# Kernel optimization log

Hardware: AMD Instinct MI355X
Metric: run time of the kernel (lower is better)

The kernel has to match this reference:

```python
import jax, jax.numpy as jnp
import numpy as np

B, T, C = 4, 2048, 1024
H, D = 16, 64  # num_heads, head_dim
SCALE = D ** -0.5


def setup_inputs() -> dict:
    key = jax.random.key(0)
    ks = jax.random.split(key, 6)
    s = 0.02
    return {
        "hidden_states": jax.random.normal(ks[0], (B, T, C), dtype=jnp.float32),
        "wq": jax.random.normal(ks[1], (C, C), dtype=jnp.float32) * s,
        "wk": jax.random.normal(ks[2], (C, C), dtype=jnp.float32) * s,
        "wv": jax.random.normal(ks[3], (C, C), dtype=jnp.float32) * s,
        "wo": jax.random.normal(ks[4], (C, C), dtype=jnp.float32) * s,
        "bo": jnp.zeros((C,), dtype=jnp.float32),
    }


def reference(hidden_states, wq, wk, wv, wo, bo):
    b, t, c = hidden_states.shape
    # torch nn.Linear: y = x @ W^T
    q = hidden_states @ wq.T
    k = hidden_states @ wk.T
    v = hidden_states @ wv.T
    # (b, t, c) -> (b, h, t, d)
    q = q.reshape(b, t, H, D).transpose(0, 2, 1, 3)
    k = k.reshape(b, t, H, D).transpose(0, 2, 1, 3)
    v = v.reshape(b, t, H, D).transpose(0, 2, 1, 3)
    scores = jnp.einsum("bhqd,bhkd->bhqk", q, k) * SCALE
    attn = jax.nn.softmax(scores, axis=-1)
    out = jnp.einsum("bhqk,bhkd->bhqd", attn, v)
    out = out.transpose(0, 2, 1, 3).reshape(b, t, c)
    return out @ wo.T + bo
```

## Files before the change

### kernel.cpp

```cpp
#include <hip/hip_runtime.h>
#include <hip/hip_bf16.h>
#include <stdint.h>
#include <math.h>

#define Bb 4
#define Tt 2048
#define Cc 1024
#define Hh 16
#define Dd 64
#define Mm (Bb * Tt)
#define KVB 64
#define NT (Tt / KVB)

typedef __attribute__((ext_vector_type(8))) short bf8;
typedef __attribute__((ext_vector_type(4))) float f32x4;
typedef __attribute__((ext_vector_type(16))) float f32x16;
typedef __attribute__((ext_vector_type(8))) float f32x8v;
typedef __attribute__((ext_vector_type(2))) float f32x2v;
typedef __attribute__((ext_vector_type(8))) unsigned short u16x8;

#define QSCALE 0.1803368801111244f
#define M_FIX 4.0f

__device__ __forceinline__ unsigned short f2bf(float f) {
  __hip_bfloat16 h = __float2bfloat16(f);
  return *reinterpret_cast<unsigned short*>(&h);
}
__device__ __forceinline__ float bf2f(unsigned short s) {
  union { unsigned u; float f; } v; v.u = ((unsigned)s) << 16;
  return v.f;
}
__device__ __forceinline__ float fexp2(float x) {
#if __has_builtin(__builtin_amdgcn_exp2f)
  return __builtin_amdgcn_exp2f(x);
#else
  return exp2f(x);
#endif
}
__device__ __forceinline__ unsigned cvtpk(float lo, float hi) {
  unsigned r;
  asm volatile("v_cvt_pk_bf16_f32 %0, %1, %2" : "=v"(r) : "v"(lo), "v"(hi));
  return r;
}
__device__ __forceinline__ void gl_lds16(const void* g, void* l) {
  __builtin_amdgcn_global_load_lds(
      (const __attribute__((address_space(1))) void*)g,
      (__attribute__((address_space(3))) void*)l, 16, 0, 0);
}

__global__ __launch_bounds__(256) void cast_all(
    const float* __restrict__ hs, const float* __restrict__ wq,
    const float* __restrict__ wk, const float* __restrict__ wv,
    const float* __restrict__ wo, unsigned short* __restrict__ Xb,
    unsigned short* __restrict__ Wbase) {
  long long g = (long long)(blockIdx.x * 256 + threadIdx.x) * 8;
  const float* src;
  unsigned short* dst;
  long long off;
  const long long HS = 8LL * 1024 * 1024;
  if (g < HS) {
    src = hs; dst = Xb; off = g;
  } else {
    long long r = g - HS;
    int wsel = (int)(r >> 20);
    off = r & ((1LL << 20) - 1);
    src = (wsel == 0) ? wq : (wsel == 1) ? wk : (wsel == 2) ? wv : wo;
    dst = Wbase + ((long long)wsel << 20);
  }
  const float4* p = (const float4*)(src + off);
  float4 a = p[0], b = p[1];
  u16x8 o;
  o[0] = f2bf(a.x); o[1] = f2bf(a.y); o[2] = f2bf(a.z); o[3] = f2bf(a.w);
  o[4] = f2bf(b.x); o[5] = f2bf(b.y); o[6] = f2bf(b.z); o[7] = f2bf(b.w);
  *(u16x8*)(dst + off) = o;
}

template <int MODE>
__global__ __launch_bounds__(256, 2)
void gemm_bt(const unsigned short* __restrict__ A,
             const unsigned short* __restrict__ Bw,
             void* __restrict__ Cout,
             const float* __restrict__ bias,
             int M, int N, int K) {
  __shared__ unsigned short smem[3 * 8192];
  const int tid = threadIdx.x;
  const int lane = tid & 63;
  const int w = tid >> 6;
  const int wr = w >> 1, wc = w & 1;
  const int row0 = blockIdx.y * 128;
  const int col0 = blockIdx.x * 128;
  const int lr = lane & 15;
  const int lk = (lane >> 4) * 8;

  f32x4 acc[4][4] = {};

  const int sr = tid >> 2;
  const int sc = (tid & 3) * 8;
  const int NK = K >> 5;

  const unsigned short* a0p = A  + (size_t)(row0 + sr) * K + sc;
  const unsigned short* a1p = A  + (size_t)(row0 + 64 + sr) * K + sc;
  const unsigned short* b0p = Bw + (size_t)(col0 + sr) * K + sc;
  const unsigned short* b1p = Bw + (size_t)(col0 + 64 + sr) * K + sc;

#define STAGE(kt, buf)                                                   \
  {                                                                      \
    unsigned short* As_ = &smem[(buf) * 8192];                           \
    unsigned short* Bs_ = &smem[(buf) * 8192 + 4096];                    \
    const int k0_ = (kt) * 32;                                           \
    gl_lds16(a0p + k0_, &As_[sr * 32 + sc]);                             \
    gl_lds16(a1p + k0_, &As_[(64 + sr) * 32 + sc]);                      \
    gl_lds16(b0p + k0_, &Bs_[sr * 32 + sc]);                             \
    gl_lds16(b1p + k0_, &Bs_[(64 + sr) * 32 + sc]);                      \
  }

  STAGE(0, 0)
  STAGE(1, 1)
  asm volatile("s_waitcnt vmcnt(4)" ::: "memory");
  __builtin_amdgcn_sched_barrier(0);
  __builtin_amdgcn_s_barrier();
  __builtin_amdgcn_sched_barrier(0);

  int cur = 0;
  for (int t = 0; t < NK; ++t) {
    if (t + 2 < NK) {
      int nb = cur + 2; if (nb >= 3) nb -= 3;
      STAGE(t + 2, nb)
    }
    const unsigned short* As_ = &smem[cur * 8192];
    const unsigned short* Bs_ = &smem[cur * 8192 + 4096];

    bf8 a[4], b[4];
#pragma unroll
    for (int mi = 0; mi < 4; ++mi)
      a[mi] = *(const bf8*)&As_[(wr * 64 + mi * 16 + lr) * 32 + lk];
#pragma unroll
    for (int ni = 0; ni < 4; ++ni)
      b[ni] = *(const bf8*)&Bs_[(wc * 64 + ni * 16 + lr) * 32 + lk];
    __builtin_amdgcn_s_setprio(1);
#pragma unroll
    for (int mi = 0; mi < 4; ++mi)
#pragma unroll
      for (int ni = 0; ni < 4; ++ni)
        acc[mi][ni] = __builtin_amdgcn_mfma_f32_16x16x32_bf16(
            a[mi], b[ni], acc[mi][ni], 0, 0, 0);
    __builtin_amdgcn_s_setprio(0);

    if (t + 2 < NK) {
      asm volatile("s_waitcnt vmcnt(4)" ::: "memory");
    } else {
      asm volatile("s_waitcnt vmcnt(0)" ::: "memory");
    }
    __builtin_amdgcn_sched_barrier(0);
    __builtin_amdgcn_s_barrier();
    __builtin_amdgcn_sched_barrier(0);
    cur = cur + 1; if (cur >= 3) cur -= 3;
  }
#undef STAGE

#pragma unroll
  for (int mi = 0; mi < 4; ++mi) {
#pragma unroll
    for (int ni = 0; ni < 4; ++ni) {
      const int col = col0 + wc * 64 + ni * 16 + lr;
      const int rowb = row0 + wr * 64 + mi * 16 + (lane >> 4) * 4;
      if (MODE == 1) {
#pragma unroll
        for (int r = 0; r < 4; ++r)
          ((float*)Cout)[(size_t)(rowb + r) * N + col] = acc[mi][ni][r] + bias[col];
      } else {
        unsigned short* outb = (unsigned short*)Cout;
        if (col < 2048) {
          unsigned short* dst = outb + (col < 1024 ? 0 : 8 * 1024 * 1024);
          const int c = col & 1023;
#pragma unroll
          for (int r = 0; r < 4; ++r)
            dst[(size_t)(rowb + r) * 1024 + c] = f2bf(acc[mi][ni][r]);
        } else {
          const int c = col - 2048;
          const int bidx = rowb >> 11, t0 = rowb & 2047;
          const int hh = c >> 6, dd = c & 63;
          uint2 pk;
          pk.x = (unsigned)f2bf(acc[mi][ni][0]) | ((unsigned)f2bf(acc[mi][ni][1]) << 16);
          pk.y = (unsigned)f2bf(acc[mi][ni][2]) | ((unsigned)f2bf(acc[mi][ni][3]) << 16);
          size_t addr = (((size_t)(bidx * Hh + hh)) * Dd + dd) * (size_t)Tt + t0;
          *(uint2*)(outb + 16 * 1024 * 1024 + addr) = pk;
        }
      }
    }
  }
}

__global__ __launch_bounds__(512, 2)
void flash_attn(const unsigned short* __restrict__ Q,
                const unsigned short* __restrict__ Km,
                const unsigned short* __restrict__ Vt,
                unsigned short* __restrict__ O) {
  __shared__ unsigned short smem[3 * 8192];

  const int tid = threadIdx.x;
  const int lane = tid & 63;
  const int w = tid >> 6;
  const int bh = blockIdx.x;
  const int qt = blockIdx.y;
  const int b = bh >> 4, h = bh & 15;
  const size_t base = (size_t)b * Tt * Cc + (size_t)h * Dd;
  const size_t vtbase = (size_t)bh * Dd * Tt;
  const int r31 = lane & 31, hi = lane >> 5;
  const int qrow = qt * 256 + w * 32 + r31;
  const int sw = r31 & 7;

  int coh[4];
#pragma unroll
  for (int ks = 0; ks < 4; ++ks) coh[ks] = ((2 * ks + hi) ^ sw) * 8;

  bf8 qb[4];
#pragma unroll
  for (int ks = 0; ks < 4; ++ks) {
    bf8 t = *(const bf8*)(Q + base + (size_t)qrow * Cc + ks * 16 + hi * 8);
#pragma unroll
    for (int i = 0; i < 8; ++i)
      qb[ks][i] = (short)f2bf(bf2f((unsigned short)t[i]) * QSCALE);
  }

  float l_r = 0.f;
  f32x16 o_acc[2];
#pragma unroll
  for (int dt = 0; dt < 2; ++dt) o_acc[dt] = (f32x16)0.0f;

  const int strow = tid >> 3;
  const int stch = tid & 7;
  const unsigned short* ksrc = Km + base + (size_t)strow * Cc + ((stch ^ (strow & 7)) * 8);
  const unsigned short* vsrc = Vt + vtbase + (size_t)strow * Tt + ((stch ^ (strow & 7)) * 8);

  gl_lds16(ksrc,                   &smem[0 * 8192 + tid * 8]);
  gl_lds16(vsrc,                   &smem[0 * 8192 + 4096 + tid * 8]);
  gl_lds16(ksrc + (size_t)KVB * Cc, &smem[1 * 8192 + tid * 8]);
  gl_lds16(vsrc + KVB,             &smem[1 * 8192 + 4096 + tid * 8]);
  asm volatile("s_waitcnt vmcnt(2)" ::: "memory");
  __builtin_amdgcn_sched_barrier(0);
  __builtin_amdgcn_s_barrier();
  __builtin_amdgcn_sched_barrier(0);

  int cur = 0;
  for (int t = 0; t < NT; ++t) {
    if (t + 2 < NT) {
      int nb = cur + 2; if (nb >= 3) nb -= 3;
      const int kb = (t + 2) * KVB;
      gl_lds16(ksrc + (size_t)kb * Cc, &smem[nb * 8192 + tid * 8]);
      gl_lds16(vsrc + kb,              &smem[nb * 8192 + 4096 + tid * 8]);
    }

    const unsigned short* ksl = &smem[cur * 8192];
    const unsigned short* vsl = &smem[cur * 8192 + 4096];

    f32x16 s0 = (f32x16)0.0f, s1 = (f32x16)0.0f;
    __builtin_amdgcn_s_setprio(1);
#pragma unroll
    for (int ks = 0; ks < 4; ++ks) {
      bf8 kf = *(const bf8*)&ksl[r31 * 64 + coh[ks]];
      s0 = __builtin_amdgcn_mfma_f32_32x32x16_bf16(kf, qb[ks], s0, 0, 0, 0);
    }
#pragma unroll
    for (int ks = 0; ks < 4; ++ks) {
      bf8 kf = *(const bf8*)&ksl[(32 + r31) * 64 + coh[ks]];
      s1 = __builtin_amdgcn_mfma_f32_32x32x16_bf16(kf, qb[ks], s1, 0, 0, 0);
    }
    __builtin_amdgcn_s_setprio(0);

    s0 = s0 - M_FIX;
    s1 = s1 - M_FIX;
#pragma unroll
    for (int j = 0; j < 16; ++j) { s0[j] = fexp2(s0[j]); s1[j] = fexp2(s1[j]); }
    {
      f32x16 t16 = s0 + s1;
      f32x8v t8v = __builtin_shufflevector(t16, t16, 0, 1, 2, 3, 4, 5, 6, 7) +
                   __builtin_shufflevector(t16, t16, 8, 9, 10, 11, 12, 13, 14, 15);
      f32x4 t4v = __builtin_shufflevector(t8v, t8v, 0, 1, 2, 3) +
                  __builtin_shufflevector(t8v, t8v, 4, 5, 6, 7);
      f32x2v t2v = __builtin_shufflevector(t4v, t4v, 0, 1) +
                   __builtin_shufflevector(t4v, t4v, 2, 3);
      float ps = t2v[0] + t2v[1];
      ps += __shfl_xor(ps, 32);
      l_r += ps;
    }

    unsigned U[8][2];
#pragma unroll
    for (int k = 0; k < 4; ++k) {
      U[k][0] = cvtpk(s0[4 * k],     s0[4 * k + 1]);
      U[k][1] = cvtpk(s0[4 * k + 2], s0[4 * k + 3]);
      U[4 + k][0] = cvtpk(s1[4 * k],     s1[4 * k + 1]);
      U[4 + k][1] = cvtpk(s1[4 * k + 2], s1[4 * k + 3]);
    }
    bf8 pb[4];
#pragma unroll
    for (int ks = 0; ks < 4; ++ks) {
      unsigned a0 = U[2 * ks][0], b0 = U[2 * ks + 1][0];
      asm volatile("v_permlane32_swap_b32 %0, %1" : "+v"(a0), "+v"(b0));
      unsigned a1 = U[2 * ks][1], b1 = U[2 * ks + 1][1];
      asm volatile("v_permlane32_swap_b32 %0, %1" : "+v"(a1), "+v"(b1));
      union { unsigned u[4]; bf8 v; } pk_;
      pk_.u[0] = a0; pk_.u[1] = a1; pk_.u[2] = b0; pk_.u[3] = b1;
      pb[ks] = pk_.v;
    }

    __builtin_amdgcn_s_setprio(1);
#pragma unroll
    for (int dt = 0; dt < 2; ++dt) {
      f32x16 z = o_acc[dt];
#pragma unroll
      for (int ks = 0; ks < 4; ++ks) {
        bf8 vf = *(const bf8*)&vsl[(dt * 32 + r31) * 64 + coh[ks]];
        z = __builtin_amdgcn_mfma_f32_32x32x16_bf16(vf, pb[ks], z, 0, 0, 0);
      }
      o_acc[dt] = z;
    }
    __builtin_amdgcn_s_setprio(0);

    if (t + 2 < NT) {
      asm volatile("s_waitcnt vmcnt(2)" ::: "memory");
    } else {
      asm volatile("s_waitcnt vmcnt(0)" ::: "memory");
    }
    __builtin_amdgcn_sched_barrier(0);
    __builtin_amdgcn_s_barrier();
    __builtin_amdgcn_sched_barrier(0);
    cur = cur + 1; if (cur >= 3) cur -= 3;
  }

  const float linv = 1.0f / l_r;
#pragma unroll
  for (int dt = 0; dt < 2; ++dt) {
    f32x16 on = o_acc[dt] * linv;
#pragma unroll
    for (int g = 0; g < 4; ++g) {
      uint2 pk;
      pk.x = (unsigned)f2bf(on[4 * g]) | ((unsigned)f2bf(on[4 * g + 1]) << 16);
      pk.y = (unsigned)f2bf(on[4 * g + 2]) | ((unsigned)f2bf(on[4 * g + 3]) << 16);
      *(uint2*)(O + base + (size_t)qrow * Cc + dt * 32 + g * 8 + hi * 4) = pk;
    }
  }
}

extern "C" void kernel_launch(void* const* d_in, const int* in_sizes, int n_in,
                              void* d_out, int out_size, void* d_ws, size_t ws_size,
                              hipStream_t stream) {
  (void)in_sizes; (void)n_in; (void)out_size; (void)ws_size;
  const float* hs = (const float*)d_in[0];
  const float* wq = (const float*)d_in[1];
  const float* wk = (const float*)d_in[2];
  const float* wv = (const float*)d_in[3];
  const float* wo = (const float*)d_in[4];
  const float* bo = (const float*)d_in[5];

  char* ws = (char*)d_ws;
  const size_t MB = 1u << 20;
  unsigned short* Xb  = (unsigned short*)(ws + 0);
  unsigned short* Wqb = (unsigned short*)(ws + 16 * MB);
  unsigned short* Wob = (unsigned short*)(ws + 22 * MB);
  unsigned short* Qb  = (unsigned short*)(ws + 24 * MB);
  unsigned short* Kb  = (unsigned short*)(ws + 40 * MB);
  unsigned short* Vtb = (unsigned short*)(ws + 56 * MB);
  unsigned short* Ob  = Xb;

  cast_all<<<6144, 256, 0, stream>>>(hs, wq, wk, wv, wo, Xb, Wqb);

  gemm_bt<3><<<dim3(24, 64), 256, 0, stream>>>(Xb, Wqb, Qb, nullptr, Mm, 3072, Cc);

  flash_attn<<<dim3(Bb * Hh, Tt / 256), 512, 0, stream>>>(Qb, Kb, Vtb, Ob);

  gemm_bt<1><<<dim3(8, 64), 256, 0, stream>>>(Ob, Wob, (float*)d_out, bo, Mm, Cc, Cc);
}
```

Measured before the change: 188.8 us.

## Process KV tiles in pairs with four-slot LDS ring and half the barriers

Restructures the flash-attention main loop to prefetch two KV tiles at once into a four-slot LDS ring and process two tiles per iteration, synchronising only once per pair. This is meant to halve barrier and waitcnt overhead and give the loads a whole pair of tiles of compute to hide behind. In exchange LDS use grows from 48KB to 64KB per block, which may limit two blocks per CU, and the wait is now a full vmcnt(0) before each barrier.

```diff
diff --git a/kernel.cpp b/kernel.cpp
--- a/kernel.cpp
+++ b/kernel.cpp
@@ -11,6 +11,7 @@
 #define Mm (Bb * Tt)
 #define KVB 64
 #define NT (Tt / KVB)
+#define NP (NT / 2)
 
 typedef __attribute__((ext_vector_type(8))) short bf8;
 typedef __attribute__((ext_vector_type(4))) float f32x4;
@@ -196,7 +197,7 @@
                 const unsigned short* __restrict__ Km,
                 const unsigned short* __restrict__ Vt,
                 unsigned short* __restrict__ O) {
-  __shared__ unsigned short smem[3 * 8192];
+  __shared__ unsigned short smem[4 * 8192];
 
   const int tid = threadIdx.x;
   const int lane = tid & 63;
@@ -233,101 +234,103 @@
   const unsigned short* ksrc = Km + base + (size_t)strow * Cc + ((stch ^ (strow & 7)) * 8);
   const unsigned short* vsrc = Vt + vtbase + (size_t)strow * Tt + ((stch ^ (strow & 7)) * 8);
 
-  gl_lds16(ksrc,                   &smem[0 * 8192 + tid * 8]);
-  gl_lds16(vsrc,                   &smem[0 * 8192 + 4096 + tid * 8]);
-  gl_lds16(ksrc + (size_t)KVB * Cc, &smem[1 * 8192 + tid * 8]);
-  gl_lds16(vsrc + KVB,             &smem[1 * 8192 + 4096 + tid * 8]);
-  asm volatile("s_waitcnt vmcnt(2)" ::: "memory");
+#define ISSUE(t)                                                          \
+  {                                                                       \
+    const int kb_ = (t) * KVB;                                            \
+    unsigned short* bp_ = &smem[((t) & 3) * 8192];                        \
+    gl_lds16(ksrc + (size_t)kb_ * Cc, bp_ + tid * 8);                     \
+    gl_lds16(vsrc + kb_,              bp_ + 4096 + tid * 8);              \
+  }
+
+#define TILE(tile)                                                            \
+  {                                                                           \
+    const unsigned short* ksl = &smem[((tile) & 3) * 8192];                   \
+    const unsigned short* vsl = ksl + 4096;                                   \
+    f32x16 s0 = (f32x16)0.0f, s1 = (f32x16)0.0f;                              \
+    __builtin_amdgcn_s_setprio(1);                                            \
+    _Pragma("unroll")                                                         \
+    for (int ks = 0; ks < 4; ++ks) {                                          \
+      bf8 kf = *(const bf8*)&ksl[r31 * 64 + coh[ks]];                         \
+      s0 = __builtin_amdgcn_mfma_f32_32x32x16_bf16(kf, qb[ks], s0, 0, 0, 0);  \
+    }                                                                         \
+    _Pragma("unroll")                                                         \
+    for (int ks = 0; ks < 4; ++ks) {                                          \
+      bf8 kf = *(const bf8*)&ksl[(32 + r31) * 64 + coh[ks]];                  \
+      s1 = __builtin_amdgcn_mfma_f32_32x32x16_bf16(kf, qb[ks], s1, 0, 0, 0);  \
+    }                                                                         \
+    __builtin_amdgcn_s_setprio(0);                                            \
+    s0 = s0 - M_FIX;                                                          \
+    s1 = s1 - M_FIX;                                                          \
+    _Pragma("unroll")                                                         \
+    for (int j = 0; j < 16; ++j) { s0[j] = fexp2(s0[j]); s1[j] = fexp2(s1[j]); } \
+    {                                                                         \
+      f32x16 t16 = s0 + s1;                                                   \
+      f32x8v t8v = __builtin_shufflevector(t16, t16, 0, 1, 2, 3, 4, 5, 6, 7) + \
+                   __builtin_shufflevector(t16, t16, 8, 9, 10, 11, 12, 13, 14, 15); \
+      f32x4 t4v = __builtin_shufflevector(t8v, t8v, 0, 1, 2, 3) +             \
+                  __builtin_shufflevector(t8v, t8v, 4, 5, 6, 7);              \
+      f32x2v t2v = __builtin_shufflevector(t4v, t4v, 0, 1) +                  \
+                   __builtin_shufflevector(t4v, t4v, 2, 3);                   \
+      float ps = t2v[0] + t2v[1];                                             \
+      ps += __shfl_xor(ps, 32);                                               \
+      l_r += ps;                                                              \
+    }                                                                         \
+    unsigned U[8][2];                                                         \
+    _Pragma("unroll")                                                         \
+    for (int k = 0; k < 4; ++k) {                                             \
+      U[k][0] = cvtpk(s0[4 * k], s0[4 * k + 1]);                              \
+      U[k][1] = cvtpk(s0[4 * k + 2], s0[4 * k + 3]);                          \
+      U[4 + k][0] = cvtpk(s1[4 * k], s1[4 * k + 1]);                          \
+      U[4 + k][1] = cvtpk(s1[4 * k + 2], s1[4 * k + 3]);                      \
+    }                                                                         \
+    bf8 pb[4];                                                                \
+    _Pragma("unroll")                                                         \
+    for (int ks = 0; ks < 4; ++ks) {                                          \
+      unsigned a0 = U[2 * ks][0], b0 = U[2 * ks + 1][0];                      \
+      asm volatile("v_permlane32_swap_b32 %0, %1" : "+v"(a0), "+v"(b0));      \
+      unsigned a1 = U[2 * ks][1], b1 = U[2 * ks + 1][1];                      \
+      asm volatile("v_permlane32_swap_b32 %0, %1" : "+v"(a1), "+v"(b1));      \
+      union { unsigned u[4]; bf8 v; } pk_;                                    \
+      pk_.u[0] = a0; pk_.u[1] = a1; pk_.u[2] = b0; pk_.u[3] = b1;             \
+      pb[ks] = pk_.v;                                                         \
+    }                                                                         \
+    __builtin_amdgcn_s_setprio(1);                                            \
+    _Pragma("unroll")                                                         \
+    for (int dt = 0; dt < 2; ++dt) {                                          \
+      f32x16 z = o_acc[dt];                                                   \
+      _Pragma("unroll")                                                       \
+      for (int ks = 0; ks < 4; ++ks) {                                        \
+        bf8 vf = *(const bf8*)&vsl[(dt * 32 + r31) * 64 + coh[ks]];           \
+        z = __builtin_amdgcn_mfma_f32_32x32x16_bf16(vf, pb[ks], z, 0, 0, 0);  \
+      }                                                                       \
+      o_acc[dt] = z;                                                          \
+    }                                                                         \
+    __builtin_amdgcn_s_setprio(0);                                            \
+  }
+
+  ISSUE(0)
+  ISSUE(1)
+  asm volatile("s_waitcnt vmcnt(0)" ::: "memory");
   __builtin_amdgcn_sched_barrier(0);
   __builtin_amdgcn_s_barrier();
   __builtin_amdgcn_sched_barrier(0);
 
-  int cur = 0;
-  for (int t = 0; t < NT; ++t) {
-    if (t + 2 < NT) {
-      int nb = cur + 2; if (nb >= 3) nb -= 3;
-      const int kb = (t + 2) * KVB;
-      gl_lds16(ksrc + (size_t)kb * Cc, &smem[nb * 8192 + tid * 8]);
-      gl_lds16(vsrc + kb,              &smem[nb * 8192 + 4096 + tid * 8]);
-    }
-
-    const unsigned short* ksl = &smem[cur * 8192];
-    const unsigned short* vsl = &smem[cur * 8192 + 4096];
-
-    f32x16 s0 = (f32x16)0.0f, s1 = (f32x16)0.0f;
-    __builtin_amdgcn_s_setprio(1);
-#pragma unroll
-    for (int ks = 0; ks < 4; ++ks) {
-      bf8 kf = *(const bf8*)&ksl[r31 * 64 + coh[ks]];
-      s0 = __builtin_amdgcn_mfma_f32_32x32x16_bf16(kf, qb[ks], s0, 0, 0, 0);
-    }
-#pragma unroll
-    for (int ks = 0; ks < 4; ++ks) {
-      bf8 kf = *(const bf8*)&ksl[(32 + r31) * 64 + coh[ks]];
-      s1 = __builtin_amdgcn_mfma_f32_32x32x16_bf16(kf, qb[ks], s1, 0, 0, 0);
-    }
-    __builtin_amdgcn_s_setprio(0);
-
-    s0 = s0 - M_FIX;
-    s1 = s1 - M_FIX;
-#pragma unroll
-    for (int j = 0; j < 16; ++j) { s0[j] = fexp2(s0[j]); s1[j] = fexp2(s1[j]); }
-    {
-      f32x16 t16 = s0 + s1;
-      f32x8v t8v = __builtin_shufflevector(t16, t16, 0, 1, 2, 3, 4, 5, 6, 7) +
-                   __builtin_shufflevector(t16, t16, 8, 9, 10, 11, 12, 13, 14, 15);
-      f32x4 t4v = __builtin_shufflevector(t8v, t8v, 0, 1, 2, 3) +
-                  __builtin_shufflevector(t8v, t8v, 4, 5, 6, 7);
-      f32x2v t2v = __builtin_shufflevector(t4v, t4v, 0, 1) +
-                   __builtin_shufflevector(t4v, t4v, 2, 3);
-      float ps = t2v[0] + t2v[1];
-      ps += __shfl_xor(ps, 32);
-      l_r += ps;
-    }
-
-    unsigned U[8][2];
-#pragma unroll
-    for (int k = 0; k < 4; ++k) {
-      U[k][0] = cvtpk(s0[4 * k],     s0[4 * k + 1]);
-      U[k][1] = cvtpk(s0[4 * k + 2], s0[4 * k + 3]);
-      U[4 + k][0] = cvtpk(s1[4 * k],     s1[4 * k + 1]);
-      U[4 + k][1] = cvtpk(s1[4 * k + 2], s1[4 * k + 3]);
-    }
-    bf8 pb[4];
-#pragma unroll
-    for (int ks = 0; ks < 4; ++ks) {
-      unsigned a0 = U[2 * ks][0], b0 = U[2 * ks + 1][0];
-      asm volatile("v_permlane32_swap_b32 %0, %1" : "+v"(a0), "+v"(b0));
-      unsigned a1 = U[2 * ks][1], b1 = U[2 * ks + 1][1];
-      asm volatile("v_permlane32_swap_b32 %0, %1" : "+v"(a1), "+v"(b1));
-      union { unsigned u[4]; bf8 v; } pk_;
-      pk_.u[0] = a0; pk_.u[1] = a1; pk_.u[2] = b0; pk_.u[3] = b1;
-      pb[ks] = pk_.v;
-    }
-
-    __builtin_amdgcn_s_setprio(1);
-#pragma unroll
-    for (int dt = 0; dt < 2; ++dt) {
-      f32x16 z = o_acc[dt];
-#pragma unroll
-      for (int ks = 0; ks < 4; ++ks) {
-        bf8 vf = *(const bf8*)&vsl[(dt * 32 + r31) * 64 + coh[ks]];
-        z = __builtin_amdgcn_mfma_f32_32x32x16_bf16(vf, pb[ks], z, 0, 0, 0);
-      }
-      o_acc[dt] = z;
-    }
-    __builtin_amdgcn_s_setprio(0);
-
-    if (t + 2 < NT) {
-      asm volatile("s_waitcnt vmcnt(2)" ::: "memory");
-    } else {
+  for (int p = 0; p < NP; ++p) {
+    if (p + 1 < NP) {
+      ISSUE(2 * p + 2)
+      ISSUE(2 * p + 3)
+    }
+    TILE(2 * p)
+    TILE(2 * p + 1)
+    if (p + 1 < NP) {
       asm volatile("s_waitcnt vmcnt(0)" ::: "memory");
-    }
-    __builtin_amdgcn_sched_barrier(0);
-    __builtin_amdgcn_s_barrier();
-    __builtin_amdgcn_sched_barrier(0);
-    cur = cur + 1; if (cur >= 3) cur -= 3;
-  }
+      __builtin_amdgcn_sched_barrier(0);
+      __builtin_amdgcn_s_barrier();
+      __builtin_amdgcn_sched_barrier(0);
+    }
+  }
+#undef TILE
+#undef ISSUE
 
   const float linv = 1.0f / l_r;
 #pragma unroll
```

After: 183.6 us. 1.03x faster.
